# Kernel tuning notes

Measured on AMD Instinct MI355X. Metric: run time of the kernel, lower is better.

Reference implementation:

```python
import jax, jax.numpy as jnp
import numpy as np

N_NODES = 50000
IN_FEATS = 256
OUT_DIM = 64
N_EDGES = 800000


def setup_inputs() -> dict:
    key = jax.random.key(0)
    k1, k2, k3, k4 = jax.random.split(key, 4)
    x = jax.random.normal(k1, (N_NODES, IN_FEATS), dtype=jnp.float32)
    edge_index = jax.random.randint(k2, (2, N_EDGES), 0, N_NODES, dtype=jnp.int64)
    # Glorot-style init for the GCN weight, zeros bias (as in PyG GCNConv)
    scale = jnp.sqrt(6.0 / (IN_FEATS + OUT_DIM)).astype(jnp.float32)
    W = jax.random.uniform(k3, (IN_FEATS, OUT_DIM), dtype=jnp.float32, minval=-1.0, maxval=1.0) * scale
    b = jnp.zeros((OUT_DIM,), dtype=jnp.float32)
    return {"x": x, "edge_index": edge_index, "W": W, "b": b}


def _gcn_relu(x, edge_index, W, b):
    n = x.shape[0]
    # linear transform first (PyG GCNConv): h = x @ W
    h = x @ W  # [N, out_dim]
    # add self-loops
    loops = jnp.arange(n, dtype=edge_index.dtype)
    src = jnp.concatenate([edge_index[0], loops])  # [E+N]
    dst = jnp.concatenate([edge_index[1], loops])
    # symmetric degree normalization: deg over target index with unit weights
    deg = jax.ops.segment_sum(jnp.ones_like(dst, dtype=h.dtype), dst, num_segments=n)
    deg_inv_sqrt = jnp.where(deg > 0, jax.lax.rsqrt(jnp.maximum(deg, 1e-12)), 0.0)
    norm = deg_inv_sqrt[src] * deg_inv_sqrt[dst]  # [E+N]
    # gather source features, scale, scatter-add at destination
    msg = h[src] * norm[:, None]  # [E+N, out_dim]
    agg = jax.ops.segment_sum(msg, dst, num_segments=n)  # [N, out_dim]
    return jax.nn.relu(agg + b)


def reference(x, edge_index, W, b):
    return _gcn_relu(x, edge_index, W, b)
```

## Files before the change

### kernel.cpp

```cpp
#include <hip/hip_runtime.h>
#include <hip/hip_fp16.h>

#define INF    256
#define OUTF   64
#define TSH    7
#define TNODE  128
#define NBMAX  512
#define CAP    3584
#define MS_T   1024
#define MS_EPT 4

typedef __attribute__((ext_vector_type(8))) short bf16x8;
typedef __attribute__((ext_vector_type(4))) float f32x4;

__device__ __forceinline__ short f2bf(float f) {
    union { float f; unsigned int u; } v; v.f = f;
    unsigned int u = v.u;
    u += 0x7FFFu + ((u >> 16) & 1u);
    return (short)(u >> 16);
}

__global__ void init_gcur_kernel(int* __restrict__ gcur, int nbuck) {
    int i = blockIdx.x * blockDim.x + threadIdx.x;
    if (i < nbuck) gcur[i] = i * CAP;
}

__global__ __launch_bounds__(MS_T) void msplit_kernel(
    const int* __restrict__ src, const int* __restrict__ dst,
    int* __restrict__ gcur, int* __restrict__ ebuk, int e, int nbuck)
{
    __shared__ int h[NBMAX], lb[NBMAX];
    const int t = threadIdx.x;
    for (int i = t; i < nbuck; i += MS_T) h[i] = 0;
    __syncthreads();

    const int base = blockIdx.x * (MS_T * MS_EPT);
    const int i0 = base + t * MS_EPT;
    int sv[MS_EPT], dl[MS_EPT], off[MS_EPT], bk[MS_EPT];

    if (i0 + MS_EPT <= e) {
        int4 s0 = *reinterpret_cast<const int4*>(src + i0);
        int4 d0 = *reinterpret_cast<const int4*>(dst + i0);
        sv[0]=s0.x; sv[1]=s0.y; sv[2]=s0.z; sv[3]=s0.w;
        int dd[MS_EPT] = {d0.x,d0.y,d0.z,d0.w};
        #pragma unroll
        for (int k = 0; k < MS_EPT; ++k) {
            bk[k] = dd[k] >> TSH; dl[k] = dd[k] & (TNODE - 1);
            off[k] = atomicAdd(&h[bk[k]], 1);
        }
    } else {
        #pragma unroll
        for (int k = 0; k < MS_EPT; ++k) {
            int i = i0 + k;
            if (i < e) {
                int dd = dst[i];
                sv[k] = src[i]; bk[k] = dd >> TSH; dl[k] = dd & (TNODE - 1);
                off[k] = atomicAdd(&h[bk[k]], 1);
            } else bk[k] = -1;
        }
    }
    __syncthreads();
    for (int i = t; i < nbuck; i += MS_T) lb[i] = h[i] ? atomicAdd(&gcur[i], h[i]) : 0;
    __syncthreads();
    #pragma unroll
    for (int k = 0; k < MS_EPT; ++k) {
        if (bk[k] >= 0) {
            int pos = lb[bk[k]] + off[k];
            if (pos < (bk[k] + 1) * CAP)
                ebuk[pos] = (sv[k] & 0xFFFF) | (dl[k] << 16);
        }
    }
}

__global__ __launch_bounds__(512) void place_kernel(
    const int* __restrict__ gcur, const int* __restrict__ ebuk,
    unsigned short* __restrict__ ecol, int* __restrict__ rowptr,
    unsigned short* __restrict__ pcnt, float* __restrict__ dinv, int n)
{
    __shared__ int h[TNODE];
    __shared__ int lcur[TNODE];
    __shared__ unsigned short outb[CAP];

    const int b = blockIdx.x;
    const int t = threadIdx.x;
    const int nb0 = b << TSH;
    const int nn  = min(TNODE, n - nb0);
    const int beg = b * CAP;
    const int m   = min(gcur[b] - beg, CAP);

    if (t < TNODE) h[t] = 0;
    __syncthreads();
    for (int i = t; i < m; i += 512)
        atomicAdd(&h[(ebuk[beg + i] >> 16) & (TNODE - 1)], 1);
    __syncthreads();

    int v = (t < TNODE) ? h[t] : 0;
    if (t < TNODE) lcur[t] = v;
    __syncthreads();
    #pragma unroll
    for (int o = 1; o < TNODE; o <<= 1) {
        int add = (t < TNODE && t >= o) ? lcur[t - o] : 0;
        __syncthreads();
        if (t < TNODE) lcur[t] += add;
        __syncthreads();
    }
    if (t < TNODE) {
        int excl = lcur[t] - v;
        if (t < nn) {
            rowptr[nb0 + t] = beg + excl;
            pcnt[nb0 + t]   = (unsigned short)v;
            dinv[nb0 + t]   = rsqrtf((float)(v + 1));
        }
        lcur[t] = excl;
    }
    __syncthreads();

    for (int i = t; i < m; i += 512) {
        int p = ebuk[beg + i];
        int o = atomicAdd(&lcur[(p >> 16) & (TNODE - 1)], 1);
        outb[o] = (unsigned short)(p & 0xFFFF);
    }
    __syncthreads();
    for (int i = t; i < m; i += 512) ecol[beg + i] = outb[i];
}

__global__ __launch_bounds__(256, 2) void gemm_mfma_kernel(
    const float* __restrict__ x, const float* __restrict__ W,
    const float* __restrict__ dinv, __half* __restrict__ hp16,
    int n, int ntiles, int wstride)
{
    __shared__ char smem[65536];
    const int lane = threadIdx.x & 63;
    const int wv   = threadIdx.x >> 6;
    const int wid  = blockIdx.x * 4 + wv;
    const int lg   = lane >> 4;
    const int lr   = lane & 15;
    char* buf0 = smem + wv * 16384;
    char* buf1 = buf0 + 8192;

    bf16x8 breg[4][8];
    #pragma unroll
    for (int ct = 0; ct < 4; ++ct) {
        #pragma unroll
        for (int ks = 0; ks < 8; ++ks) {
            const float* wp = W + (size_t)(ks * 32 + lg * 8) * OUTF + ct * 16 + lr;
            bf16x8 f;
            #pragma unroll
            for (int j = 0; j < 8; ++j)
                f[j] = f2bf(wp[(size_t)j * OUTF]);
            breg[ct][ks] = f;
        }
    }

    auto stage_half = [&](const float* xrow0, char* buf) {
        #pragma unroll
        for (int i = 0; i < 8; ++i) {
            int row  = i * 2 + (lane >> 5);
            int colb = (((lane & 31) << 4) ^ ((row & 7) << 4));
            const float* srcp = xrow0 + (size_t)row * INF + (colb >> 2);
            __builtin_amdgcn_global_load_lds(
                (const __attribute__((address_space(1))) void*)srcp,
                (__attribute__((address_space(3))) void*)(buf + i * 1024),
                16, 0, 0);
        }
        asm volatile("" ::: "memory");
    };

    auto compute_half = [&](const char* buf, int khbase,
                            f32x4& acc0, f32x4& acc1, f32x4& acc2, f32x4& acc3) {
        const int m = (lr & 7) << 4;
        #pragma unroll
        for (int ksl = 0; ksl < 4; ++ksl) {
            int logical = lr * 512 + ksl * 128 + lg * 32;
            float4 a0 = *reinterpret_cast<const float4*>(buf + (logical ^ m));
            float4 a1 = *reinterpret_cast<const float4*>(buf + ((logical + 16) ^ m));
            bf16x8 af;
            af[0] = f2bf(a0.x); af[1] = f2bf(a0.y); af[2] = f2bf(a0.z); af[3] = f2bf(a0.w);
            af[4] = f2bf(a1.x); af[5] = f2bf(a1.y); af[6] = f2bf(a1.z); af[7] = f2bf(a1.w);
            acc0 = __builtin_amdgcn_mfma_f32_16x16x32_bf16(af, breg[0][khbase + ksl], acc0, 0, 0, 0);
            acc1 = __builtin_amdgcn_mfma_f32_16x16x32_bf16(af, breg[1][khbase + ksl], acc1, 0, 0, 0);
            acc2 = __builtin_amdgcn_mfma_f32_16x16x32_bf16(af, breg[2][khbase + ksl], acc2, 0, 0, 0);
            acc3 = __builtin_amdgcn_mfma_f32_16x16x32_bf16(af, breg[3][khbase + ksl], acc3, 0, 0, 0);
        }
    };

    for (int t = wid; t < ntiles; t += wstride) {
        const float* xt = x + (size_t)t * 16 * INF;
        stage_half(xt, buf0);
        stage_half(xt + 128, buf1);

        f32x4 acc0 = {0,0,0,0}, acc1 = {0,0,0,0}, acc2 = {0,0,0,0}, acc3 = {0,0,0,0};

        asm volatile("s_waitcnt vmcnt(8)" ::: "memory");
        compute_half(buf0, 0, acc0, acc1, acc2, acc3);

        asm volatile("s_waitcnt vmcnt(0)" ::: "memory");
        compute_half(buf1, 4, acc0, acc1, acc2, acc3);

        #pragma unroll
        for (int reg = 0; reg < 4; ++reg) {
            int row = t * 16 + lg * 4 + reg;
            float di = dinv[row];
            __half* op = hp16 + (size_t)row * OUTF + lr;
            op[0]  = __float2half(acc0[reg] * di);
            op[16] = __float2half(acc1[reg] * di);
            op[32] = __float2half(acc2[reg] * di);
            op[48] = __float2half(acc3[reg] * di);
        }
    }
}

__global__ __launch_bounds__(256) void aggregate_kernel(
    const int* __restrict__ rowptr, const unsigned short* __restrict__ pcnt,
    const unsigned short* __restrict__ ecol, const __half2* __restrict__ hp2,
    const float* __restrict__ dinv, const float* __restrict__ b,
    float* __restrict__ out, int n)
{
    int widx = (int)((blockIdx.x * (size_t)blockDim.x + threadIdx.x) >> 6);
    int lane = threadIdx.x & 63;
    int half = lane >> 5;
    int l    = lane & 31;
    if (widx >= n) return;

    float2 acc = make_float2(0.f, 0.f);
    if (half == 0) {
        float2 v = __half22float2(hp2[(size_t)widx * 32 + l]);
        acc.x = v.x; acc.y = v.y;
    }

    int beg = rowptr[widx];
    int end = beg + pcnt[widx];

    int j = beg + half;
    for (; j + 14 < end; j += 16) {
        int s0 = ecol[j];      int s1 = ecol[j + 2];
        int s2 = ecol[j + 4];  int s3 = ecol[j + 6];
        int s4 = ecol[j + 8];  int s5 = ecol[j + 10];
        int s6 = ecol[j + 12]; int s7 = ecol[j + 14];
        float2 v0 = __half22float2(hp2[(size_t)s0 * 32 + l]);
        float2 v1 = __half22float2(hp2[(size_t)s1 * 32 + l]);
        float2 v2 = __half22float2(hp2[(size_t)s2 * 32 + l]);
        float2 v3 = __half22float2(hp2[(size_t)s3 * 32 + l]);
        float2 v4 = __half22float2(hp2[(size_t)s4 * 32 + l]);
        float2 v5 = __half22float2(hp2[(size_t)s5 * 32 + l]);
        float2 v6 = __half22float2(hp2[(size_t)s6 * 32 + l]);
        float2 v7 = __half22float2(hp2[(size_t)s7 * 32 + l]);
        acc.x += v0.x + v1.x + v2.x + v3.x + v4.x + v5.x + v6.x + v7.x;
        acc.y += v0.y + v1.y + v2.y + v3.y + v4.y + v5.y + v6.y + v7.y;
    }
    for (; j < end; j += 2) {
        float2 v = __half22float2(hp2[(size_t)ecol[j] * 32 + l]);
        acc.x += v.x; acc.y += v.y;
    }

    float hx = __shfl(acc.x, lane | 32, 64);
    float hy = __shfl(acc.y, lane | 32, 64);
    if (half == 0) {
        float di = dinv[widx];
        float2 bb = reinterpret_cast<const float2*>(b)[l];
        float ox = fmaxf((acc.x + hx) * di + bb.x, 0.f);
        float oy = fmaxf((acc.y + hy) * di + bb.y, 0.f);
        reinterpret_cast<float2*>(out)[(size_t)widx * 32 + l] = make_float2(ox, oy);
    }
}

extern "C" void kernel_launch(void* const* d_in, const int* in_sizes, int n_in,
                              void* d_out, int out_size, void* d_ws, size_t ws_size,
                              hipStream_t stream) {
    const float* x    = (const float*)d_in[0];
    const int*   edge = (const int*)d_in[1];
    const float* W    = (const float*)d_in[2];
    const float* b    = (const float*)d_in[3];
    float* out = (float*)d_out;

    const int n = in_sizes[0] / INF;
    const int e = in_sizes[1] / 2;
    const int* src = edge;
    const int* dst = edge + e;
    const int nbuck = (n + TNODE - 1) >> TSH;

    char* wsc = (char*)d_ws;
    size_t off = 0;
    auto alloc = [&](size_t bytes) { char* p = wsc + off; off += (bytes + 511) & ~511ull; return p; };
    int*            gcur   = (int*)   alloc((size_t)NBMAX * 4);
    int*            rowptr = (int*)   alloc((size_t)n * 4);
    unsigned short* pcnt   = (unsigned short*)alloc((size_t)n * 2);
    float*          dinv   = (float*) alloc((size_t)n * 4);
    int*            ebuk   = (int*)   alloc((size_t)nbuck * CAP * 4);
    unsigned short* ecol   = (unsigned short*)alloc((size_t)nbuck * CAP * 2);
    __half*         hp16   = (__half*)alloc((size_t)n * OUTF * 2);

    init_gcur_kernel<<<2, 256, 0, stream>>>(gcur, nbuck);

    {
        int blocks = (e + MS_T * MS_EPT - 1) / (MS_T * MS_EPT);
        msplit_kernel<<<blocks, MS_T, 0, stream>>>(src, dst, gcur, ebuk, e, nbuck);
    }

    place_kernel<<<nbuck, 512, 0, stream>>>(gcur, ebuk, ecol, rowptr, pcnt, dinv, n);

    {
        const int ntiles = (n + 15) / 16;
        const int blocks = 512;
        gemm_mfma_kernel<<<blocks, 256, 0, stream>>>(x, W, dinv, hp16, n, ntiles, blocks * 4);
    }

    aggregate_kernel<<<(n + 3) / 4, 256, 0, stream>>>(rowptr, pcnt, ecol,
        reinterpret_cast<const __half2*>(hp16), dinv, b, out, n);
}
```

Before: 74.62 us.

## Aggregate with 16-byte gathers, 8 neighbors per wave, and shuffled indices

Restructures the aggregation kernel so each wave splits into 8 groups of 8 lanes. Each group gathers a full 128-byte fp16 row of a different neighbor with 16-byte loads, and the partial sums are reduced across groups with xor shuffles. Neighbor indices are loaded once per wave with a coalesced read and spread to the groups by shuffle, instead of scalar per-edge index loads. This trades fewer, wider memory requests and more in-flight rows for extra shuffle reduction work and more accumulator registers.

```diff
diff --git a/kernel.cpp b/kernel.cpp
--- a/kernel.cpp
+++ b/kernel.cpp
@@ -18,6 +18,17 @@
     unsigned int u = v.u;
     u += 0x7FFFu + ((u >> 16) & 1u);
     return (short)(u >> 16);
+}
+
+__device__ __forceinline__ void acc_u4(float4& a, float4& bq, uint4 u) {
+    __half2 h0 = *reinterpret_cast<__half2*>(&u.x);
+    __half2 h1 = *reinterpret_cast<__half2*>(&u.y);
+    __half2 h2 = *reinterpret_cast<__half2*>(&u.z);
+    __half2 h3 = *reinterpret_cast<__half2*>(&u.w);
+    float2 f0 = __half22float2(h0), f1 = __half22float2(h1);
+    float2 f2 = __half22float2(h2), f3 = __half22float2(h3);
+    a.x  += f0.x; a.y  += f0.y; a.z  += f1.x; a.w  += f1.y;
+    bq.x += f2.x; bq.y += f2.y; bq.z += f3.x; bq.w += f3.y;
 }
 
 __global__ void init_gcur_kernel(int* __restrict__ gcur, int nbuck) {
@@ -212,55 +223,91 @@
 
 __global__ __launch_bounds__(256) void aggregate_kernel(
     const int* __restrict__ rowptr, const unsigned short* __restrict__ pcnt,
-    const unsigned short* __restrict__ ecol, const __half2* __restrict__ hp2,
+    const unsigned short* __restrict__ ecol, const uint4* __restrict__ hp4,
     const float* __restrict__ dinv, const float* __restrict__ b,
     float* __restrict__ out, int n)
 {
     int widx = (int)((blockIdx.x * (size_t)blockDim.x + threadIdx.x) >> 6);
     int lane = threadIdx.x & 63;
-    int half = lane >> 5;
-    int l    = lane & 31;
+    int q = lane >> 3;
+    int l = lane & 7;
     if (widx >= n) return;
 
-    float2 acc = make_float2(0.f, 0.f);
-    if (half == 0) {
-        float2 v = __half22float2(hp2[(size_t)widx * 32 + l]);
-        acc.x = v.x; acc.y = v.y;
-    }
-
-    int beg = rowptr[widx];
-    int end = beg + pcnt[widx];
-
-    int j = beg + half;
-    for (; j + 14 < end; j += 16) {
-        int s0 = ecol[j];      int s1 = ecol[j + 2];
-        int s2 = ecol[j + 4];  int s3 = ecol[j + 6];
-        int s4 = ecol[j + 8];  int s5 = ecol[j + 10];
-        int s6 = ecol[j + 12]; int s7 = ecol[j + 14];
-        float2 v0 = __half22float2(hp2[(size_t)s0 * 32 + l]);
-        float2 v1 = __half22float2(hp2[(size_t)s1 * 32 + l]);
-        float2 v2 = __half22float2(hp2[(size_t)s2 * 32 + l]);
-        float2 v3 = __half22float2(hp2[(size_t)s3 * 32 + l]);
-        float2 v4 = __half22float2(hp2[(size_t)s4 * 32 + l]);
-        float2 v5 = __half22float2(hp2[(size_t)s5 * 32 + l]);
-        float2 v6 = __half22float2(hp2[(size_t)s6 * 32 + l]);
-        float2 v7 = __half22float2(hp2[(size_t)s7 * 32 + l]);
-        acc.x += v0.x + v1.x + v2.x + v3.x + v4.x + v5.x + v6.x + v7.x;
-        acc.y += v0.y + v1.y + v2.y + v3.y + v4.y + v5.y + v6.y + v7.y;
-    }
-    for (; j < end; j += 2) {
-        float2 v = __half22float2(hp2[(size_t)ecol[j] * 32 + l]);
-        acc.x += v.x; acc.y += v.y;
-    }
-
-    float hx = __shfl(acc.x, lane | 32, 64);
-    float hy = __shfl(acc.y, lane | 32, 64);
-    if (half == 0) {
+    float4 accA = make_float4(0.f, 0.f, 0.f, 0.f);
+    float4 accB = make_float4(0.f, 0.f, 0.f, 0.f);
+    if (q == 0)
+        acc_u4(accA, accB, hp4[(size_t)widx * 8 + l]);
+
+    const int beg = rowptr[widx];
+    const int deg = pcnt[widx];
+    const int dcap = min(deg, 64);
+
+    int idx = (lane < deg) ? (int)ecol[beg + lane] : 0;
+
+    int k = 0;
+    for (; k + 32 <= dcap; k += 32) {
+        int s0 = __shfl(idx, k + q, 64);
+        int s1 = __shfl(idx, k + q + 8, 64);
+        int s2 = __shfl(idx, k + q + 16, 64);
+        int s3 = __shfl(idx, k + q + 24, 64);
+        uint4 u0 = hp4[(size_t)s0 * 8 + l];
+        uint4 u1 = hp4[(size_t)s1 * 8 + l];
+        uint4 u2 = hp4[(size_t)s2 * 8 + l];
+        uint4 u3 = hp4[(size_t)s3 * 8 + l];
+        acc_u4(accA, accB, u0); acc_u4(accA, accB, u1);
+        acc_u4(accA, accB, u2); acc_u4(accA, accB, u3);
+    }
+    for (; k + 16 <= dcap; k += 16) {
+        int s0 = __shfl(idx, k + q, 64);
+        int s1 = __shfl(idx, k + q + 8, 64);
+        uint4 u0 = hp4[(size_t)s0 * 8 + l];
+        uint4 u1 = hp4[(size_t)s1 * 8 + l];
+        acc_u4(accA, accB, u0); acc_u4(accA, accB, u1);
+    }
+    for (; k + 8 <= dcap; k += 8) {
+        int s0 = __shfl(idx, k + q, 64);
+        acc_u4(accA, accB, hp4[(size_t)s0 * 8 + l]);
+    }
+    {
+        int s0 = __shfl(idx, k + q, 64);
+        if (k + q < dcap)
+            acc_u4(accA, accB, hp4[(size_t)s0 * 8 + l]);
+    }
+    for (int kk = 64; kk < deg; kk += 8) {
+        if (kk + q < deg) {
+            int s0 = ecol[beg + kk + q];
+            acc_u4(accA, accB, hp4[(size_t)s0 * 8 + l]);
+        }
+    }
+
+    #pragma unroll
+    for (int mask = 8; mask <= 32; mask <<= 1) {
+        accA.x += __shfl_xor(accA.x, mask, 64);
+        accA.y += __shfl_xor(accA.y, mask, 64);
+        accA.z += __shfl_xor(accA.z, mask, 64);
+        accA.w += __shfl_xor(accA.w, mask, 64);
+        accB.x += __shfl_xor(accB.x, mask, 64);
+        accB.y += __shfl_xor(accB.y, mask, 64);
+        accB.z += __shfl_xor(accB.z, mask, 64);
+        accB.w += __shfl_xor(accB.w, mask, 64);
+    }
+
+    if (q == 0) {
         float di = dinv[widx];
-        float2 bb = reinterpret_cast<const float2*>(b)[l];
-        float ox = fmaxf((acc.x + hx) * di + bb.x, 0.f);
-        float oy = fmaxf((acc.y + hy) * di + bb.y, 0.f);
-        reinterpret_cast<float2*>(out)[(size_t)widx * 32 + l] = make_float2(ox, oy);
+        const float4* bv = reinterpret_cast<const float4*>(b);
+        float4 b0 = bv[l * 2], b1 = bv[l * 2 + 1];
+        float4 o0, o1;
+        o0.x = fmaxf(accA.x * di + b0.x, 0.f);
+        o0.y = fmaxf(accA.y * di + b0.y, 0.f);
+        o0.z = fmaxf(accA.z * di + b0.z, 0.f);
+        o0.w = fmaxf(accA.w * di + b0.w, 0.f);
+        o1.x = fmaxf(accB.x * di + b1.x, 0.f);
+        o1.y = fmaxf(accB.y * di + b1.y, 0.f);
+        o1.z = fmaxf(accB.z * di + b1.z, 0.f);
+        o1.w = fmaxf(accB.w * di + b1.w, 0.f);
+        float4* ov = reinterpret_cast<float4*>(out) + (size_t)widx * 16 + l * 2;
+        ov[0] = o0;
+        ov[1] = o1;
     }
 }
 
@@ -306,5 +353,5 @@
     }
 
     aggregate_kernel<<<(n + 3) / 4, 256, 0, stream>>>(rowptr, pcnt, ecol,
-        reinterpret_cast<const __half2*>(hp16), dinv, b, out, n);
-}
+        reinterpret_cast<const uint4*>(hp16), dinv, b, out, n);
+}
```

Measured after the change: 65.80 us (median of 2 runs). -11.8%, faster.
